# Optimization experiments

Hardware: AMD Instinct MI355X
Metric: run time of the kernel (lower is better)

Reference implementation:

```python
import jax, jax.numpy as jnp
import numpy as np

N_CLASS, N_SUPPORT, N_QUERY = 5, 5, 15
C, T, V = 128, 8, 25
LN_EPS = 1e-12


def setup_inputs() -> dict:
    key = jax.random.key(0)
    ks = jax.random.split(key, 6)
    n_tot = N_CLASS * (N_SUPPORT + N_QUERY)
    inp = jax.random.normal(ks[0], (n_tot, C, T, V), dtype=jnp.float32)
    # episode labels: 20 consecutive samples per class (arange // per_class)
    target = (jnp.arange(n_tot, dtype=jnp.int32) // (N_SUPPORT + N_QUERY)).astype(jnp.int32)
    s = 0.02
    p = lambda k: jax.random.normal(k, (C, C), dtype=jnp.float32) * s
    return {
        'input': inp,
        'Wq': p(ks[1]), 'bq': jnp.zeros((C,), jnp.float32),
        'Wk': p(ks[2]), 'bk': jnp.zeros((C,), jnp.float32),
        'Wv': p(ks[3]), 'bv': jnp.zeros((C,), jnp.float32),
        'Wo': p(ks[4]), 'bo': jnp.zeros((C,), jnp.float32),
        'ln_g': jnp.ones((C,), jnp.float32), 'ln_b': jnp.zeros((C,), jnp.float32),
        'target': target,
        'n_support': N_SUPPORT,
    }


def _layer_norm(x, g, b):
    mu = x.mean(-1, keepdims=True)
    var = ((x - mu) ** 2).mean(-1, keepdims=True)
    return (x - mu) * jax.lax.rsqrt(var + LN_EPS) * g + b


def _episode_forward(input, Wq, bq, Wk, bk, Wv, bv, Wo, bo, ln_g, ln_b, target, n_support):
    n_tot, c, t, v = input.shape
    m = N_CLASS
    per_class = n_tot // m
    n_query = per_class - n_support
    n = m * n_query

    # support/query split (stable argsort == torch.where per class for sorted labels)
    order = jnp.argsort(target).reshape(m, per_class)
    supp_idx = order[:, :n_support]                      # (m, h)
    qry_idx = order[:, n_support:].reshape(-1)           # (n,)
    z_proto = input[supp_idx]                            # (m, h, c, t, v)
    zq = input[qry_idx]                                  # (n, c, t, v)

    # ---- hal(): pairwise cross-attention over the vertex axis ----
    mh = m * n_support
    zq_p = jnp.transpose(zq, (0, 2, 3, 1))                                   # (n, t, v, c)
    zp_p = jnp.transpose(z_proto.reshape(mh, c, t, v), (0, 2, 3, 1))          # (mh, t, v, c)
    cat = jnp.concatenate([zq_p, zp_p], axis=0)                               # (n1, t, v, c)
    n1 = cat.shape[0]

    # Q from each of the n1 items, K/V from each of the mh prototypes.
    # Equivalent to the original expand->reshape pairing, without duplicating K/V.
    Q = cat @ Wq + bq                                                         # (n1, t, v, c)
    K = zp_p @ Wk + bk                                                        # (mh, t, v, c)
    Vv = zp_p @ Wv + bv                                                       # (mh, t, v, c)
    scale = 1.0 / jnp.sqrt(jnp.asarray(c, dtype=Q.dtype))
    scores = jnp.einsum('ntqc,mtkc->nmtqk', Q, K) * scale                     # (n1, mh, t, v, v)
    attn = jax.nn.softmax(scores, axis=-1)
    ctx = jnp.einsum('nmtqk,mtkc->nmtqc', attn, Vv)                           # (n1, mh, t, v, c)
    out = _layer_norm(ctx @ Wo + bo + cat[:, None], ln_g, ln_b)               # residual + LN
    att = out.mean(axis=1)                                                    # (n1, t, v, c) mean over mh pairs

    zq_att = jnp.transpose(att[:n], (0, 3, 1, 2))                             # (n, c, t, v)
    proto_att = att[n:].reshape(m, n_support, t, v, c).mean(axis=1)           # (m, t, v, c)
    proto_att = jnp.transpose(proto_att, (0, 3, 1, 2))                        # (m, c, t, v)

    # ---- squared-Euclidean metric on flattened features ----
    zq_f = zq_att.reshape(n, -1)
    zp_f = proto_att.reshape(m, -1)
    dist = jnp.sum((zq_f[:, None, :] - zp_f[None, :, :]) ** 2, axis=-1)       # (n, m)

    log_p_y = jax.nn.log_softmax(-dist, axis=1).reshape(m, n_query, m)
    cls = jnp.arange(m)
    loss = -log_p_y[cls[:, None], jnp.arange(n_query)[None, :], cls[:, None]].mean()
    y_hat = jnp.argmax(log_p_y, axis=2)
    acc = (y_hat == cls[:, None]).astype(jnp.float32).mean()
    return loss, acc


def reference(input, Wq, bq, Wk, bk, Wv, bv, Wo, bo, ln_g, ln_b, target, n_support):
    return _episode_forward(input, Wq, bq, Wk, bk, Wv, bv, Wo, bo, ln_g, ln_b, target, n_support)
```

## Files before the change

### kernel.cpp

```cpp
#include <hip/hip_runtime.h>
#include <math.h>

#define NTOT 100
#define NQ   75
#define NP   25
#define CC   128
#define TT   8
#define VV   25
#define NCLS 5
#define NSUP 5
#define NQRY 15
#define ROW  (TT*VV*CC)
#define TILE (VV*CC)
#define ROWS_Q 20000
#define ROWS_S 5000
#define RB_Q 625
#define RB_S 157

typedef __attribute__((ext_vector_type(8))) short short8;
typedef __attribute__((ext_vector_type(16))) float f32x16;

typedef union { uint4 u4; short8 s8; } pk_t;

__device__ __forceinline__ ushort f2bf(float f) {
    uint u = __float_as_uint(f);
    u += 0x7FFFu + ((u >> 16) & 1u);
    return (ushort)(u >> 16);
}
__device__ __forceinline__ float bf2f(uint u16v) {
    return __uint_as_float(u16v << 16);
}
__device__ __forceinline__ uint pkbf(float a, float b) {
    return (uint)f2bf(a) | ((uint)f2bf(b) << 16);
}

__global__ __launch_bounds__(256) void k_pack(
    const float* __restrict__ Wq, const float* __restrict__ Wk,
    const float* __restrict__ Wv, const float* __restrict__ Wo,
    const int* __restrict__ target,
    ushort* __restrict__ WfG, int* __restrict__ ordG) {
    int which = blockIdx.x;
    if (which == 4) {
        __shared__ int tg[NTOT];
        int tid = threadIdx.x;
        if (tid < NTOT) tg[tid] = target[tid];
        __syncthreads();
        if (tid < NTOT) {
            int ti = tg[tid], rank = 0;
            for (int j = 0; j < NTOT; ++j) {
                int tj = tg[j];
                rank += (tj < ti) || (tj == ti && j < tid);
            }
            ordG[rank] = tid;
        }
        return;
    }
    const float* W = (which == 0) ? Wq : (which == 1) ? Wk : (which == 2) ? Wv : Wo;
    ushort* dstbase = WfG + (size_t)which * 16384;
    for (int o = threadIdx.x; o < 2048; o += 256) {
        int k8 = o >> 7, c = o & 127;
        uint4 pk;
        pk.x = pkbf(W[(k8*8+0)*128 + c], W[(k8*8+1)*128 + c]);
        pk.y = pkbf(W[(k8*8+2)*128 + c], W[(k8*8+3)*128 + c]);
        pk.z = pkbf(W[(k8*8+4)*128 + c], W[(k8*8+5)*128 + c]);
        pk.w = pkbf(W[(k8*8+6)*128 + c], W[(k8*8+7)*128 + c]);
        int dst = (((c >> 5) * 8 + (k8 >> 1)) * 64 + ((c & 31) + 32 * (k8 & 1))) * 8;
        *(uint4*)(dstbase + dst) = pk;
    }
}

__global__ __launch_bounds__(256) void k_proj(
    const float* __restrict__ input, const int* __restrict__ ordG,
    const ushort* __restrict__ WfG,
    const float* __restrict__ bq, const float* __restrict__ bk,
    const float* __restrict__ bv,
    ushort* __restrict__ catC, ushort* __restrict__ Qf,
    ushort* __restrict__ Kf, ushort* __restrict__ Vf,
    int* __restrict__ counter) {
    __shared__ ushort stage[32 * 132];
    __shared__ ushort VtF[4096];

    int bid = blockIdx.x, tid = threadIdx.x;
    int w = tid >> 6, lane = tid & 63, half = lane >> 5, l31 = lane & 31;

    if (bid == 0 && tid == 0) *counter = 0;

    bool isQ = bid >= RB_S;
    int rowblk = isQ ? bid - RB_S : bid;
    int rlimit = isQ ? ROWS_Q : ROWS_S;
    int g0 = rowblk * 32;
    int gend = min(g0 + 32, rlimit);

    for (int nn = g0 / 200; nn <= (gend - 1) / 200; ++nn) {
        int lo = max(g0 - nn * 200, 0);
        int hi = min(gend - 1 - nn * 200, 199);
        int len = hi - lo + 1;
        int nidx = isQ ? nn : (NQ + nn);
        int src;
        if (nidx < NQ) { int m = nidx / NQRY, qq = nidx - m * NQRY; src = ordG[m * 20 + NSUP + qq]; }
        else           { int i2 = nidx - NQ; int m = i2 / NSUP, s = i2 - m * NSUP; src = ordG[m * 20 + s]; }
        const float* inb = input + (size_t)src * ROW + lo;
        int rbase = nn * 200 + lo - g0;
        int nv4 = len >> 2;
        int total4 = nv4 << 7;
        int qstep = 256 / nv4, rstep = 256 - qstep * nv4;
        int c = tid / nv4, v = tid - c * nv4;
        for (int idx = tid; idx < total4; idx += 256) {
            int k = v << 2;
            float4 f = *(const float4*)(inb + c * 200 + k);
            int ro = (rbase + k) * 132 + c;
            stage[ro]       = f2bf(f.x);
            stage[ro + 132] = f2bf(f.y);
            stage[ro + 264] = f2bf(f.z);
            stage[ro + 396] = f2bf(f.w);
            c += qstep; v += rstep;
            if (v >= nv4) { v -= nv4; ++c; }
        }
    }
    __syncthreads();

    short8 af[8];
    #pragma unroll
    for (int ks = 0; ks < 8; ++ks)
        af[ks] = *(const short8*)&stage[l31 * 132 + ks * 16 + half * 8];

    #define CHAIN(A, OUT, BASE) do {                                             \
        const ushort* bp_ = (BASE) + w * 4096 + lane * 8;                        \
        _Pragma("unroll")                                                        \
        for (int ks = 0; ks < 8; ++ks) {                                         \
            short8 bf_ = *(const short8*)(bp_ + ks * 512);                       \
            OUT = __builtin_amdgcn_mfma_f32_32x32x16_bf16(A[ks], bf_, OUT, 0, 0, 0); \
        }                                                                        \
    } while (0)

    if (isQ) {
        f32x16 Cm;
        #pragma unroll
        for (int r = 0; r < 16; ++r) Cm[r] = 0.f;
        CHAIN(af, Cm, WfG);
        float bcol = bq[w * 32 + l31];
        int c = w * 32 + l31;
        #pragma unroll
        for (int r = 0; r < 16; ++r) {
            int row = g0 + (r & 3) + 8 * (r >> 2) + 4 * half;
            int st = row / 25, vv = row - st * 25;
            size_t dst = (((size_t)st * 8 + (c >> 4)) * 64 + (vv + 32 * ((c >> 3) & 1))) * 8 + (c & 7);
            Qf[dst] = f2bf(Cm[r] + bcol);
        }
        uint* cc = (uint*)catC + (size_t)g0 * 64;
        for (int idx = tid; idx < 2048; idx += 256) {
            int row = idx >> 6, c2 = (idx & 63) * 2;
            cc[idx] = (uint)stage[row * 132 + c2] | ((uint)stage[row * 132 + c2 + 1] << 16);
        }
    } else {
        {
            f32x16 Cm;
            #pragma unroll
            for (int r = 0; r < 16; ++r) Cm[r] = 0.f;
            CHAIN(af, Cm, WfG + 16384);
            float bcol = bk[w * 32 + l31];
            int c = w * 32 + l31;
            #pragma unroll
            for (int r = 0; r < 16; ++r) {
                int row = g0 + (r & 3) + 8 * (r >> 2) + 4 * half;
                if (row < ROWS_S) {
                    int st = row / 25, vv = row - st * 25;
                    size_t dst = (((size_t)st * 8 + (c >> 4)) * 64 + (vv + 32 * ((c >> 3) & 1))) * 8 + (c & 7);
                    Kf[dst] = f2bf(Cm[r] + bcol);
                }
            }
        }
        {
            f32x16 Cm;
            #pragma unroll
            for (int r = 0; r < 16; ++r) Cm[r] = 0.f;
            CHAIN(af, Cm, WfG + 32768);
            float bcol = bv[w * 32 + l31];
            int c = w * 32 + l31;
            int ks2 = c >> 4, kh = (c >> 3) & 1, j2 = c & 7;
            #pragma unroll
            for (int r = 0; r < 16; ++r) {
                int rowLocal = (r & 3) + 8 * (r >> 2) + 4 * half;
                VtF[ks2 * 512 + (rowLocal + 32 * kh) * 8 + j2] = f2bf(Cm[r] + bcol);
            }
        }
        __syncthreads();
        short8 a2[8];
        #pragma unroll
        for (int ks = 0; ks < 8; ++ks)
            a2[ks] = *(const short8*)&VtF[ks * 512 + lane * 8];
        {
            f32x16 Cm;
            #pragma unroll
            for (int r = 0; r < 16; ++r) Cm[r] = 0.f;
            CHAIN(a2, Cm, WfG + 49152);
            int c = w * 32 + l31;
            #pragma unroll
            for (int r = 0; r < 16; ++r) {
                int row = g0 + (r & 3) + 8 * (r >> 2) + 4 * half;
                if (row < ROWS_S) {
                    int tile = row / 25, vv = row - tile * 25;
                    size_t dst = ((((size_t)tile * 4 + (c >> 5)) * 2 + (vv >> 4)) * 64
                                  + ((c & 31) + 32 * ((vv & 15) >> 3))) * 8 + (vv & 7);
                    Vf[dst] = f2bf(Cm[r]);
                }
            }
        }
    }
    #undef CHAIN
}

__global__ __launch_bounds__(256, 2) void k_attn(
    const ushort* __restrict__ Qf, const ushort* __restrict__ Kf,
    const ushort* __restrict__ Vf, const ushort* __restrict__ catC,
    const float* __restrict__ bo, float* __restrict__ att) {
    __shared__ __align__(16) char smem[26016];
    float*  catb = (float*)smem;
    ushort* qls  = (ushort*)(smem + 12912);
    float (*red)[50][65] = (float (*)[50][65])smem;

    int pair = blockIdx.x;
    int t = pair & 7;
    int tid = threadIdx.x;
    int wv = tid >> 6, lane = tid & 63;
    int q = lane & 31, half = lane >> 5;

    {
        const uint* cc = (const uint*)catC + (size_t)pair * 1600;
        for (int i2 = tid; i2 < 1600; i2 += 256) {
            uint u = cc[i2];
            int r = i2 >> 6, c2 = (i2 & 63) * 2;
            catb[r * 129 + c2]     = bf2f(u & 0xffffu) + bo[c2];
            catb[r * 129 + c2 + 1] = bf2f(u >> 16) + bo[c2 + 1];
        }
    }
    {
        const uint* qp = (const uint*)(Qf + (size_t)pair * 4096);
        uint* ql = (uint*)qls;
        for (int i2 = tid; i2 < 2048; i2 += 256) ql[i2] = qp[i2];
    }
    __syncthreads();

    int qc = q < 25 ? q : 24;
    float attsum[64];
    #pragma unroll
    for (int i = 0; i < 64; ++i) attsum[i] = 0.f;
    float Csc = 0.f;

    const float CEXP = (float)(1.4426950408889634 * 0.08838834764831845);

    const ushort* kbase = Kf + (size_t)t * 4096 + lane * 8;
    short8 kf[8];
    #pragma unroll
    for (int ks = 0; ks < 8; ++ks)
        kf[ks] = *(const short8*)(kbase + (size_t)wv * 32768 + ks * 512);

    int cnt = (wv == 0) ? 7 : 6;
    for (int mi = 0; mi < cnt; ++mi) {
        int m = wv + 4 * mi;

        f32x16 S;
        #pragma unroll
        for (int r = 0; r < 16; ++r) S[r] = 0.f;
        #pragma unroll
        for (int ks = 0; ks < 8; ++ks) {
            short8 qv = *(const short8*)(qls + ks * 512 + lane * 8);
            S = __builtin_amdgcn_mfma_f32_32x32x16_bf16(kf[ks], qv, S, 0, 0, 0);
        }

        float p[16], mx = -3e38f;
        #pragma unroll
        for (int r = 0; r < 16; ++r) {
            int key = (r & 3) + 8 * (r >> 2) + 4 * half;
            float v = (key < 25) ? S[r] : -3e38f;
            p[r] = v; mx = fmaxf(mx, v);
        }
        mx = fmaxf(mx, __shfl_xor(mx, 32));
        float sum = 0.f;
        #pragma unroll
        for (int r = 0; r < 16; ++r) { p[r] = exp2f((p[r] - mx) * CEXP); sum += p[r]; }
        sum += __shfl_xor(sum, 32);
        float inv = 1.f / sum;

        const ushort* vp = Vf + ((size_t)(m * 8 + t)) * 4096 + lane * 8;
        short8 vf0 = *(const short8*)(vp);
        short8 vf1 = *(const short8*)(vp + 512);
        short8 vf2 = *(const short8*)(vp + 1024);
        short8 vf3 = *(const short8*)(vp + 1536);
        short8 vf4 = *(const short8*)(vp + 2048);
        short8 vf5 = *(const short8*)(vp + 2560);
        short8 vf6 = *(const short8*)(vp + 3072);
        short8 vf7 = *(const short8*)(vp + 3584);
        #pragma unroll
        for (int ks = 0; ks < 8; ++ks)
            kf[ks] = *(const short8*)(kbase + (size_t)(m + 4) * 32768 + ks * 512);

        uint o01   = pkbf(p[0] * inv,  p[1] * inv);
        uint o23   = pkbf(p[2] * inv,  p[3] * inv);
        uint o45   = pkbf(p[4] * inv,  p[5] * inv);
        uint o67   = pkbf(p[6] * inv,  p[7] * inv);
        uint o89   = pkbf(p[8] * inv,  p[9] * inv);
        uint o1011 = pkbf(p[10] * inv, p[11] * inv);
        uint o1213 = pkbf(p[12] * inv, p[13] * inv);
        uint o1415 = pkbf(p[14] * inv, p[15] * inv);
        bool h0 = (half == 0);
        uint rA = __shfl_xor(h0 ? o45 : o01, 32);
        uint rB = __shfl_xor(h0 ? o67 : o23, 32);
        uint rC = __shfl_xor(h0 ? o1213 : o89, 32);
        uint rD = __shfl_xor(h0 ? o1415 : o1011, 32);
        pk_t P0, P1;
        P0.u4 = h0 ? make_uint4(o01, o23, rA, rB) : make_uint4(rA, rB, o45, o67);
        P1.u4 = h0 ? make_uint4(o89, o1011, rC, rD) : make_uint4(rC, rD, o1213, o1415);
        short8 pb0 = P0.s8, pb1 = P1.s8;

        f32x16 ctx[4];
        #pragma unroll
        for (int mt = 0; mt < 4; ++mt) {
            #pragma unroll
            for (int r = 0; r < 16; ++r) ctx[mt][r] = 0.f;
        }
        ctx[0] = __builtin_amdgcn_mfma_f32_32x32x16_bf16(vf0, pb0, ctx[0], 0, 0, 0);
        ctx[0] = __builtin_amdgcn_mfma_f32_32x32x16_bf16(vf1, pb1, ctx[0], 0, 0, 0);
        ctx[1] = __builtin_amdgcn_mfma_f32_32x32x16_bf16(vf2, pb0, ctx[1], 0, 0, 0);
        ctx[1] = __builtin_amdgcn_mfma_f32_32x32x16_bf16(vf3, pb1, ctx[1], 0, 0, 0);
        ctx[2] = __builtin_amdgcn_mfma_f32_32x32x16_bf16(vf4, pb0, ctx[2], 0, 0, 0);
        ctx[2] = __builtin_amdgcn_mfma_f32_32x32x16_bf16(vf5, pb1, ctx[2], 0, 0, 0);
        ctx[3] = __builtin_amdgcn_mfma_f32_32x32x16_bf16(vf6, pb0, ctx[3], 0, 0, 0);
        ctx[3] = __builtin_amdgcn_mfma_f32_32x32x16_bf16(vf7, pb1, ctx[3], 0, 0, 0);

        float s1 = 0.f, s2 = 0.f;
        #pragma unroll
        for (int mt = 0; mt < 4; ++mt) {
            float t1 = 0.f, t2 = 0.f;
            #pragma unroll
            for (int r = 0; r < 16; ++r) {
                int c = mt * 32 + (r & 3) + 8 * (r >> 2) + 4 * half;
                float xv = ctx[mt][r] + catb[qc * 129 + c];
                ctx[mt][r] = xv;
                t1 += xv; t2 = fmaf(xv, xv, t2);
            }
            s1 += t1; s2 += t2;
        }
        s1 += __shfl_xor(s1, 32); s2 += __shfl_xor(s2, 32);
        float mu = s1 * (1.f / 128.f);
        float var = s2 * (1.f / 128.f) - mu * mu;
        var = fmaxf(var, 0.f);
        float rs = rsqrtf(var + 1e-12f);
        #pragma unroll
        for (int i = 0; i < 64; ++i)
            attsum[i] = fmaf(ctx[i >> 4][i & 15], rs, attsum[i]);
        Csc = fmaf(-mu, rs, Csc);
    }

    __syncthreads();
    int s = half * 25 + q;
    bool act = q < 25;
    if ((wv == 1 || wv == 3) && act) {
        float (*rg)[65] = red[wv >> 1];
        #pragma unroll
        for (int i = 0; i < 64; ++i) rg[s][i] = attsum[i];
        rg[s][64] = Csc;
    }
    __syncthreads();
    if ((wv == 0 || wv == 2) && act) {
        float (*rg)[65] = red[wv >> 1];
        #pragma unroll
        for (int i = 0; i < 64; ++i) attsum[i] += rg[s][i];
        Csc += rg[s][64];
    }
    __syncthreads();
    if (wv == 2 && act) {
        #pragma unroll
        for (int i = 0; i < 64; ++i) red[0][s][i] = attsum[i];
        red[0][s][64] = Csc;
    }
    __syncthreads();
    if (wv == 0 && act) {
        #pragma unroll
        for (int i = 0; i < 64; ++i) attsum[i] += red[0][s][i];
        Csc += red[0][s][64];
        float* ap = att + (size_t)pair * TILE + q * 128;
        #pragma unroll
        for (int mt = 0; mt < 4; ++mt) {
            #pragma unroll
            for (int rg4 = 0; rg4 < 4; ++rg4) {
                int c0 = mt * 32 + 8 * rg4 + 4 * half;
                int i0 = mt * 16 + rg4 * 4;
                float4 o;
                o.x = attsum[i0 + 0] + Csc; o.y = attsum[i0 + 1] + Csc;
                o.z = attsum[i0 + 2] + Csc; o.w = attsum[i0 + 3] + Csc;
                *(float4*)&ap[c0] = o;
            }
        }
    }
}

__global__ __launch_bounds__(256) void k_proto(
    const float* __restrict__ att, float* __restrict__ proto) {
    int b = blockIdx.x;
    int j = b >> 3, chunk = b & 7;
    const float4* s0 = (const float4*)(att + (size_t)(NQ + j * 5 + 0) * ROW);
    const float4* s1 = (const float4*)(att + (size_t)(NQ + j * 5 + 1) * ROW);
    const float4* s2 = (const float4*)(att + (size_t)(NQ + j * 5 + 2) * ROW);
    const float4* s3 = (const float4*)(att + (size_t)(NQ + j * 5 + 3) * ROW);
    const float4* s4 = (const float4*)(att + (size_t)(NQ + j * 5 + 4) * ROW);
    float4* pr = (float4*)(proto + (size_t)j * ROW);
    int e0 = chunk * 800, e1 = e0 + 800;
    for (int e4 = e0 + threadIdx.x; e4 < e1; e4 += 256) {
        float4 q0 = s0[e4], q1 = s1[e4], q2 = s2[e4], q3 = s3[e4], q4 = s4[e4];
        float4 o;
        o.x = 0.2f * (q0.x + q1.x + q2.x + q3.x + q4.x);
        o.y = 0.2f * (q0.y + q1.y + q2.y + q3.y + q4.y);
        o.z = 0.2f * (q0.z + q1.z + q2.z + q3.z + q4.z);
        o.w = 0.2f * (q0.w + q1.w + q2.w + q3.w + q4.w);
        pr[e4] = o;
    }
}

__global__ __launch_bounds__(256) void k_dist_loss(
    const float* __restrict__ att, const float* __restrict__ proto,
    const float* __restrict__ ln_g,
    float* __restrict__ dist, int* __restrict__ counter,
    float* __restrict__ out) {
    int i = blockIdx.x;
    const float4* a  = (const float4*)(att + (size_t)i * ROW);
    const float4* p0 = (const float4*)(proto + (size_t)0 * ROW);
    const float4* p1 = (const float4*)(proto + (size_t)1 * ROW);
    const float4* p2 = (const float4*)(proto + (size_t)2 * ROW);
    const float4* p3 = (const float4*)(proto + (size_t)3 * ROW);
    const float4* p4 = (const float4*)(proto + (size_t)4 * ROW);
    float d0 = 0.f, d1 = 0.f, d2 = 0.f, d3 = 0.f, d4 = 0.f;
    for (int e4 = threadIdx.x; e4 < 6400; e4 += 256) {
        float4 av = a[e4];
        float4 g4 = *(const float4*)(ln_g + (e4 & 31) * 4);
        float gx = g4.x * g4.x, gy = g4.y * g4.y, gz = g4.z * g4.z, gw = g4.w * g4.w;
        #define ACC(PD, DD) do {                                              \
            float4 pv = PD[e4];                                               \
            float dx = av.x - pv.x, dy = av.y - pv.y;                         \
            float dz = av.z - pv.z, dw = av.w - pv.w;                         \
            DD = fmaf(gx, dx * dx, DD);                                       \
            DD = fmaf(gy, dy * dy, DD);                                       \
            DD = fmaf(gz, dz * dz, DD);                                       \
            DD = fmaf(gw, dw * dw, DD);                                       \
        } while (0)
        ACC(p0, d0); ACC(p1, d1); ACC(p2, d2); ACC(p3, d3); ACC(p4, d4);
        #undef ACC
    }
    #pragma unroll
    for (int msk = 32; msk >= 1; msk >>= 1) {
        d0 += __shfl_xor(d0, msk);
        d1 += __shfl_xor(d1, msk);
        d2 += __shfl_xor(d2, msk);
        d3 += __shfl_xor(d3, msk);
        d4 += __shfl_xor(d4, msk);
    }
    __shared__ float part[4][5];
    __shared__ int lastFlag;
    int lane = threadIdx.x & 63, wv = threadIdx.x >> 6;
    if (lane == 0) {
        part[wv][0] = d0; part[wv][1] = d1; part[wv][2] = d2;
        part[wv][3] = d3; part[wv][4] = d4;
    }
    __syncthreads();
    if (threadIdx.x == 0) {
        #pragma unroll
        for (int j = 0; j < 5; ++j) {
            float total = (part[0][j] + part[1][j] + part[2][j] + part[3][j]) * (1.f / 625.f);
            __hip_atomic_store(&dist[i * 5 + j], total, __ATOMIC_RELEASE, __HIP_MEMORY_SCOPE_AGENT);
        }
        int tk = __hip_atomic_fetch_add(counter, 1, __ATOMIC_ACQ_REL, __HIP_MEMORY_SCOPE_AGENT);
        lastFlag = (tk == 74);
    }
    __syncthreads();
    if (!lastFlag) return;

    int iq = threadIdx.x;
    float li = 0.f, ok = 0.f;
    if (iq < NQ) {
        float dd[5];
        #pragma unroll
        for (int jj = 0; jj < 5; ++jj)
            dd[jj] = __hip_atomic_load(&dist[iq * 5 + jj], __ATOMIC_ACQUIRE, __HIP_MEMORY_SCOPE_AGENT);
        int cls = iq / NQRY;
        float mind = dd[0];
        int best = 0;
        #pragma unroll
        for (int jj = 1; jj < 5; ++jj) {
            if (dd[jj] < mind) mind = dd[jj];
            if (dd[jj] < dd[best]) best = jj;
        }
        float sume = 0.f;
        #pragma unroll
        for (int jj = 0; jj < 5; ++jj) sume += expf(mind - dd[jj]);
        float lse = logf(sume) - mind;
        li = dd[cls] + lse;
        ok = (best == cls) ? 1.f : 0.f;
    }
    #pragma unroll
    for (int msk = 32; msk >= 1; msk >>= 1) {
        li += __shfl_xor(li, msk);
        ok += __shfl_xor(ok, msk);
    }
    if (lane == 0) { part[wv][0] = li; part[wv][1] = ok; }
    __syncthreads();
    if (threadIdx.x == 0) {
        out[0] = (part[0][0] + part[1][0] + part[2][0] + part[3][0]) / 75.f;
        out[1] = (part[0][1] + part[1][1] + part[2][1] + part[3][1]) / 75.f;
    }
}

extern "C" void kernel_launch(void* const* d_in, const int* in_sizes, int n_in,
                              void* d_out, int out_size, void* d_ws, size_t ws_size,
                              hipStream_t stream) {
    const float* input = (const float*)d_in[0];
    const float* Wq   = (const float*)d_in[1];
    const float* bq   = (const float*)d_in[2];
    const float* Wk   = (const float*)d_in[3];
    const float* bk   = (const float*)d_in[4];
    const float* Wv   = (const float*)d_in[5];
    const float* bv   = (const float*)d_in[6];
    const float* Wo   = (const float*)d_in[7];
    const float* bo   = (const float*)d_in[8];
    const float* ln_g = (const float*)d_in[9];
    const float* ln_b = (const float*)d_in[10];
    const int* target = (const int*)d_in[11];
    float* out = (float*)d_out;
    (void)ln_b;

    float* ws = (float*)d_ws;
    ushort* catC = (ushort*)ws;
    ushort* Qf   = catC + 2560000;
    ushort* Kf   = Qf + 3276800;
    ushort* Vf   = Kf + 819200;
    float*  att  = (float*)(Vf + 819200);
    float*  distb = att + 2560000;
    int*    counter = (int*)(distb + 512);
    ushort* WfG  = (ushort*)(counter + 16);
    int*    ordG = (int*)(WfG + 65536);
    float*  proto = (float*)catC;

    k_pack<<<5, 256, 0, stream>>>(Wq, Wk, Wv, Wo, target, WfG, ordG);
    k_proj<<<RB_Q + RB_S, 256, 0, stream>>>(input, ordG, WfG, bq, bk, bv,
                                            catC, Qf, Kf, Vf, counter);
    k_attn<<<800, 256, 0, stream>>>(Qf, Kf, Vf, catC, bo, att);
    k_proto<<<40, 256, 0, stream>>>(att, proto);
    k_dist_loss<<<75, 256, 0, stream>>>(att, proto, ln_g, distb, counter, out);
}
```

Measured before the change: 170.1 us.

## Accumulate attention sums via LDS atomics and drop K-fragment prefetch

Each wave now adds its normalized context contributions into a shared-memory accumulator with atomicAdd, replacing the 64-register per-thread accumulator and the multi-step cross-wave tree reduction. K fragments are loaded at the top of each iteration instead of prefetched for the next one, and the final tile is written cooperatively by all threads. This frees registers, aiming at higher occupancy, but adds many LDS atomics per iteration, exposes K load latency, and raises LDS use per block.

```diff
diff --git a/kernel.cpp b/kernel.cpp
--- a/kernel.cpp
+++ b/kernel.cpp
@@ -214,10 +214,11 @@
     const ushort* __restrict__ Qf, const ushort* __restrict__ Kf,
     const ushort* __restrict__ Vf, const ushort* __restrict__ catC,
     const float* __restrict__ bo, float* __restrict__ att) {
-    __shared__ __align__(16) char smem[26016];
-    float*  catb = (float*)smem;
-    ushort* qls  = (ushort*)(smem + 12912);
-    float (*red)[50][65] = (float (*)[50][65])smem;
+    __shared__ __align__(16) char smem[37744];
+    float*  catb   = (float*)smem;
+    ushort* qls    = (ushort*)(smem + 12912);
+    float*  attacc = (float*)(smem + 21104);
+    float*  cscacc = attacc + 32 * 129;
 
     int pair = blockIdx.x;
     int t = pair & 7;
@@ -239,25 +240,24 @@
         uint* ql = (uint*)qls;
         for (int i2 = tid; i2 < 2048; i2 += 256) ql[i2] = qp[i2];
     }
+    for (int i2 = tid; i2 < 32 * 129 + 32; i2 += 256) attacc[i2] = 0.f;
     __syncthreads();
 
     int qc = q < 25 ? q : 24;
-    float attsum[64];
-    #pragma unroll
-    for (int i = 0; i < 64; ++i) attsum[i] = 0.f;
-    float Csc = 0.f;
+    bool act = q < 25;
 
     const float CEXP = (float)(1.4426950408889634 * 0.08838834764831845);
 
     const ushort* kbase = Kf + (size_t)t * 4096 + lane * 8;
-    short8 kf[8];
-    #pragma unroll
-    for (int ks = 0; ks < 8; ++ks)
-        kf[ks] = *(const short8*)(kbase + (size_t)wv * 32768 + ks * 512);
 
     int cnt = (wv == 0) ? 7 : 6;
     for (int mi = 0; mi < cnt; ++mi) {
         int m = wv + 4 * mi;
+
+        short8 kf[8];
+        #pragma unroll
+        for (int ks = 0; ks < 8; ++ks)
+            kf[ks] = *(const short8*)(kbase + (size_t)m * 32768 + ks * 512);
 
         f32x16 S;
         #pragma unroll
@@ -291,9 +291,6 @@
         short8 vf5 = *(const short8*)(vp + 2560);
         short8 vf6 = *(const short8*)(vp + 3072);
         short8 vf7 = *(const short8*)(vp + 3584);
-        #pragma unroll
-        for (int ks = 0; ks < 8; ++ks)
-            kf[ks] = *(const short8*)(kbase + (size_t)(m + 4) * 32768 + ks * 512);
 
         uint o01   = pkbf(p[0] * inv,  p[1] * inv);
         uint o23   = pkbf(p[2] * inv,  p[3] * inv);
@@ -346,51 +343,31 @@
         float var = s2 * (1.f / 128.f) - mu * mu;
         var = fmaxf(var, 0.f);
         float rs = rsqrtf(var + 1e-12f);
-        #pragma unroll
-        for (int i = 0; i < 64; ++i)
-            attsum[i] = fmaf(ctx[i >> 4][i & 15], rs, attsum[i]);
-        Csc = fmaf(-mu, rs, Csc);
+
+        if (act) {
+            float* arow = attacc + q * 129;
+            #pragma unroll
+            for (int mt = 0; mt < 4; ++mt) {
+                #pragma unroll
+                for (int r = 0; r < 16; ++r) {
+                    int c = mt * 32 + (r & 3) + 8 * (r >> 2) + 4 * half;
+                    atomicAdd(&arow[c], ctx[mt][r] * rs);
+                }
+            }
+            if (h0) atomicAdd(&cscacc[q], -mu * rs);
+        }
     }
 
     __syncthreads();
-    int s = half * 25 + q;
-    bool act = q < 25;
-    if ((wv == 1 || wv == 3) && act) {
-        float (*rg)[65] = red[wv >> 1];
-        #pragma unroll
-        for (int i = 0; i < 64; ++i) rg[s][i] = attsum[i];
-        rg[s][64] = Csc;
-    }
-    __syncthreads();
-    if ((wv == 0 || wv == 2) && act) {
-        float (*rg)[65] = red[wv >> 1];
-        #pragma unroll
-        for (int i = 0; i < 64; ++i) attsum[i] += rg[s][i];
-        Csc += rg[s][64];
-    }
-    __syncthreads();
-    if (wv == 2 && act) {
-        #pragma unroll
-        for (int i = 0; i < 64; ++i) red[0][s][i] = attsum[i];
-        red[0][s][64] = Csc;
-    }
-    __syncthreads();
-    if (wv == 0 && act) {
-        #pragma unroll
-        for (int i = 0; i < 64; ++i) attsum[i] += red[0][s][i];
-        Csc += red[0][s][64];
-        float* ap = att + (size_t)pair * TILE + q * 128;
-        #pragma unroll
-        for (int mt = 0; mt < 4; ++mt) {
-            #pragma unroll
-            for (int rg4 = 0; rg4 < 4; ++rg4) {
-                int c0 = mt * 32 + 8 * rg4 + 4 * half;
-                int i0 = mt * 16 + rg4 * 4;
-                float4 o;
-                o.x = attsum[i0 + 0] + Csc; o.y = attsum[i0 + 1] + Csc;
-                o.z = attsum[i0 + 2] + Csc; o.w = attsum[i0 + 3] + Csc;
-                *(float4*)&ap[c0] = o;
-            }
+    {
+        float* ap = att + (size_t)pair * TILE;
+        for (int idx = tid; idx < 800; idx += 256) {
+            int qq = idx >> 5, c4 = (idx & 31) * 4;
+            float cs = cscacc[qq];
+            const float* ar = attacc + qq * 129 + c4;
+            float4 o;
+            o.x = ar[0] + cs; o.y = ar[1] + cs; o.z = ar[2] + cs; o.w = ar[3] + cs;
+            *(float4*)&ap[qq * 128 + c4] = o;
         }
     }
 }
```

Result: slower. 549.7 us (+223.1%).

## Fuse Q projection and input staging into attention kernel

Applied to the files above, without the earlier changes.

The Q projection and the bf16 staging of each (item, t) tile move from k_proj into k_attn, which now reads the fp32 input directly, transposes it into shared memory, and computes Q with MFMA locally. k_proj now handles only the support rows (K, V and the Wo-folded V), so its grid shrinks from 782 to 157 blocks. This removes the global round-trip of the Qf and catC intermediates. In exchange k_attn uses more shared memory and does an uncoalesced strided transpose load from the input for each block.

```diff
diff --git a/kernel.cpp b/kernel.cpp
--- a/kernel.cpp
+++ b/kernel.cpp
@@ -12,9 +12,7 @@
 #define NQRY 15
 #define ROW  (TT*VV*CC)
 #define TILE (VV*CC)
-#define ROWS_Q 20000
 #define ROWS_S 5000
-#define RB_Q 625
 #define RB_S 157
 
 typedef __attribute__((ext_vector_type(8))) short short8;
@@ -72,9 +70,7 @@
 __global__ __launch_bounds__(256) void k_proj(
     const float* __restrict__ input, const int* __restrict__ ordG,
     const ushort* __restrict__ WfG,
-    const float* __restrict__ bq, const float* __restrict__ bk,
-    const float* __restrict__ bv,
-    ushort* __restrict__ catC, ushort* __restrict__ Qf,
+    const float* __restrict__ bk, const float* __restrict__ bv,
     ushort* __restrict__ Kf, ushort* __restrict__ Vf,
     int* __restrict__ counter) {
     __shared__ ushort stage[32 * 132];
@@ -85,20 +81,15 @@
 
     if (bid == 0 && tid == 0) *counter = 0;
 
-    bool isQ = bid >= RB_S;
-    int rowblk = isQ ? bid - RB_S : bid;
-    int rlimit = isQ ? ROWS_Q : ROWS_S;
-    int g0 = rowblk * 32;
-    int gend = min(g0 + 32, rlimit);
+    int g0 = bid * 32;
+    int gend = min(g0 + 32, ROWS_S);
 
     for (int nn = g0 / 200; nn <= (gend - 1) / 200; ++nn) {
         int lo = max(g0 - nn * 200, 0);
         int hi = min(gend - 1 - nn * 200, 199);
         int len = hi - lo + 1;
-        int nidx = isQ ? nn : (NQ + nn);
-        int src;
-        if (nidx < NQ) { int m = nidx / NQRY, qq = nidx - m * NQRY; src = ordG[m * 20 + NSUP + qq]; }
-        else           { int i2 = nidx - NQ; int m = i2 / NSUP, s = i2 - m * NSUP; src = ordG[m * 20 + s]; }
+        int m = nn / NSUP, s = nn - m * NSUP;
+        int src = ordG[m * 20 + s];
         const float* inb = input + (size_t)src * ROW + lo;
         int rbase = nn * 200 + lo - g0;
         int nv4 = len >> 2;
@@ -133,111 +124,119 @@
         }                                                                        \
     } while (0)
 
-    if (isQ) {
+    {
         f32x16 Cm;
         #pragma unroll
         for (int r = 0; r < 16; ++r) Cm[r] = 0.f;
-        CHAIN(af, Cm, WfG);
-        float bcol = bq[w * 32 + l31];
+        CHAIN(af, Cm, WfG + 16384);
+        float bcol = bk[w * 32 + l31];
         int c = w * 32 + l31;
         #pragma unroll
         for (int r = 0; r < 16; ++r) {
             int row = g0 + (r & 3) + 8 * (r >> 2) + 4 * half;
-            int st = row / 25, vv = row - st * 25;
-            size_t dst = (((size_t)st * 8 + (c >> 4)) * 64 + (vv + 32 * ((c >> 3) & 1))) * 8 + (c & 7);
-            Qf[dst] = f2bf(Cm[r] + bcol);
-        }
-        uint* cc = (uint*)catC + (size_t)g0 * 64;
-        for (int idx = tid; idx < 2048; idx += 256) {
-            int row = idx >> 6, c2 = (idx & 63) * 2;
-            cc[idx] = (uint)stage[row * 132 + c2] | ((uint)stage[row * 132 + c2 + 1] << 16);
-        }
-    } else {
-        {
-            f32x16 Cm;
-            #pragma unroll
-            for (int r = 0; r < 16; ++r) Cm[r] = 0.f;
-            CHAIN(af, Cm, WfG + 16384);
-            float bcol = bk[w * 32 + l31];
-            int c = w * 32 + l31;
-            #pragma unroll
-            for (int r = 0; r < 16; ++r) {
-                int row = g0 + (r & 3) + 8 * (r >> 2) + 4 * half;
-                if (row < ROWS_S) {
-                    int st = row / 25, vv = row - st * 25;
-                    size_t dst = (((size_t)st * 8 + (c >> 4)) * 64 + (vv + 32 * ((c >> 3) & 1))) * 8 + (c & 7);
-                    Kf[dst] = f2bf(Cm[r] + bcol);
-                }
+            if (row < ROWS_S) {
+                int st = row / 25, vv = row - st * 25;
+                size_t dst = (((size_t)st * 8 + (c >> 4)) * 64 + (vv + 32 * ((c >> 3) & 1))) * 8 + (c & 7);
+                Kf[dst] = f2bf(Cm[r] + bcol);
             }
         }
-        {
-            f32x16 Cm;
-            #pragma unroll
-            for (int r = 0; r < 16; ++r) Cm[r] = 0.f;
-            CHAIN(af, Cm, WfG + 32768);
-            float bcol = bv[w * 32 + l31];
-            int c = w * 32 + l31;
-            int ks2 = c >> 4, kh = (c >> 3) & 1, j2 = c & 7;
-            #pragma unroll
-            for (int r = 0; r < 16; ++r) {
-                int rowLocal = (r & 3) + 8 * (r >> 2) + 4 * half;
-                VtF[ks2 * 512 + (rowLocal + 32 * kh) * 8 + j2] = f2bf(Cm[r] + bcol);
+    }
+    {
+        f32x16 Cm;
+        #pragma unroll
+        for (int r = 0; r < 16; ++r) Cm[r] = 0.f;
+        CHAIN(af, Cm, WfG + 32768);
+        float bcol = bv[w * 32 + l31];
+        int c = w * 32 + l31;
+        int ks2 = c >> 4, kh = (c >> 3) & 1, j2 = c & 7;
+        #pragma unroll
+        for (int r = 0; r < 16; ++r) {
+            int rowLocal = (r & 3) + 8 * (r >> 2) + 4 * half;
+            VtF[ks2 * 512 + (rowLocal + 32 * kh) * 8 + j2] = f2bf(Cm[r] + bcol);
+        }
+    }
+    __syncthreads();
+    short8 a2[8];
+    #pragma unroll
+    for (int ks = 0; ks < 8; ++ks)
+        a2[ks] = *(const short8*)&VtF[ks * 512 + lane * 8];
+    {
+        f32x16 Cm;
+        #pragma unroll
+        for (int r = 0; r < 16; ++r) Cm[r] = 0.f;
+        CHAIN(a2, Cm, WfG + 49152);
+        int c = w * 32 + l31;
+        #pragma unroll
+        for (int r = 0; r < 16; ++r) {
+            int row = g0 + (r & 3) + 8 * (r >> 2) + 4 * half;
+            if (row < ROWS_S) {
+                int tile = row / 25, vv = row - tile * 25;
+                size_t dst = ((((size_t)tile * 4 + (c >> 5)) * 2 + (vv >> 4)) * 64
+                              + ((c & 31) + 32 * ((vv & 15) >> 3))) * 8 + (vv & 7);
+                Vf[dst] = f2bf(Cm[r]);
             }
         }
-        __syncthreads();
-        short8 a2[8];
-        #pragma unroll
-        for (int ks = 0; ks < 8; ++ks)
-            a2[ks] = *(const short8*)&VtF[ks * 512 + lane * 8];
-        {
-            f32x16 Cm;
-            #pragma unroll
-            for (int r = 0; r < 16; ++r) Cm[r] = 0.f;
-            CHAIN(a2, Cm, WfG + 49152);
-            int c = w * 32 + l31;
-            #pragma unroll
-            for (int r = 0; r < 16; ++r) {
-                int row = g0 + (r & 3) + 8 * (r >> 2) + 4 * half;
-                if (row < ROWS_S) {
-                    int tile = row / 25, vv = row - tile * 25;
-                    size_t dst = ((((size_t)tile * 4 + (c >> 5)) * 2 + (vv >> 4)) * 64
-                                  + ((c & 31) + 32 * ((vv & 15) >> 3))) * 8 + (vv & 7);
-                    Vf[dst] = f2bf(Cm[r]);
-                }
-            }
-        }
     }
     #undef CHAIN
 }
 
 __global__ __launch_bounds__(256, 2) void k_attn(
-    const ushort* __restrict__ Qf, const ushort* __restrict__ Kf,
-    const ushort* __restrict__ Vf, const ushort* __restrict__ catC,
+    const float* __restrict__ input, const int* __restrict__ ordG,
+    const ushort* __restrict__ WfG, const float* __restrict__ bq,
+    const ushort* __restrict__ Kf, const ushort* __restrict__ Vf,
     const float* __restrict__ bo, float* __restrict__ att) {
-    __shared__ __align__(16) char smem[26016];
-    float*  catb = (float*)smem;
-    ushort* qls  = (ushort*)(smem + 12912);
+    __shared__ __align__(16) char smem[29552];
+    float*  catb  = (float*)smem;
+    ushort* qls   = (ushort*)(smem + 12912);
+    ushort* stage = (ushort*)(smem + 21104);
     float (*red)[50][65] = (float (*)[50][65])smem;
 
     int pair = blockIdx.x;
-    int t = pair & 7;
+    int t = pair & 7, n = pair >> 3;
     int tid = threadIdx.x;
     int wv = tid >> 6, lane = tid & 63;
-    int q = lane & 31, half = lane >> 5;
-
+    int q = lane & 31, half = lane >> 5, l31 = lane & 31;
+
+    int src;
+    if (n < NQ) { int m = n / NQRY, qq = n - m * NQRY; src = ordG[m * 20 + NSUP + qq]; }
+    else        { int i2 = n - NQ; int m = i2 / NSUP, s = i2 - m * NSUP; src = ordG[m * 20 + s]; }
+
+    for (int idx = tid; idx < 7 * 132; idx += 256) stage[3300 + idx] = 0;
     {
-        const uint* cc = (const uint*)catC + (size_t)pair * 1600;
-        for (int i2 = tid; i2 < 1600; i2 += 256) {
-            uint u = cc[i2];
-            int r = i2 >> 6, c2 = (i2 & 63) * 2;
-            catb[r * 129 + c2]     = bf2f(u & 0xffffu) + bo[c2];
-            catb[r * 129 + c2 + 1] = bf2f(u >> 16) + bo[c2 + 1];
-        }
+        const float* inb = input + (size_t)src * ROW + t * 25;
+        for (int idx = tid; idx < 3200; idx += 256) {
+            int c = idx / 25, v = idx - c * 25;
+            stage[v * 132 + c] = f2bf(inb[c * 200 + v]);
+        }
+    }
+    __syncthreads();
+
+    for (int idx = tid; idx < 3200; idx += 256) {
+        int r = idx >> 7, c2 = idx & 127;
+        catb[r * 129 + c2] = bf2f((uint)stage[r * 132 + c2]) + bo[c2];
     }
     {
-        const uint* qp = (const uint*)(Qf + (size_t)pair * 4096);
-        uint* ql = (uint*)qls;
-        for (int i2 = tid; i2 < 2048; i2 += 256) ql[i2] = qp[i2];
+        short8 af[8];
+        #pragma unroll
+        for (int ks = 0; ks < 8; ++ks)
+            af[ks] = *(const short8*)&stage[l31 * 132 + ks * 16 + half * 8];
+        f32x16 Cm;
+        #pragma unroll
+        for (int r = 0; r < 16; ++r) Cm[r] = 0.f;
+        const ushort* bp = WfG + wv * 4096 + lane * 8;
+        #pragma unroll
+        for (int ks = 0; ks < 8; ++ks) {
+            short8 bf_ = *(const short8*)(bp + ks * 512);
+            Cm = __builtin_amdgcn_mfma_f32_32x32x16_bf16(af[ks], bf_, Cm, 0, 0, 0);
+        }
+        float bcol = bq[wv * 32 + l31];
+        int c = wv * 32 + l31;
+        int ks2 = c >> 4, kh = (c >> 3) & 1, j2 = c & 7;
+        #pragma unroll
+        for (int r = 0; r < 16; ++r) {
+            int rowLocal = (r & 3) + 8 * (r >> 2) + 4 * half;
+            qls[ks2 * 512 + (rowLocal + 32 * kh) * 8 + j2] = f2bf(Cm[r] + bcol);
+        }
     }
     __syncthreads();
 
@@ -528,21 +527,18 @@
     (void)ln_b;
 
     float* ws = (float*)d_ws;
-    ushort* catC = (ushort*)ws;
-    ushort* Qf   = catC + 2560000;
-    ushort* Kf   = Qf + 3276800;
+    float*  proto = (float*)ws;
+    ushort* Kf   = (ushort*)(proto + 5 * ROW);
     ushort* Vf   = Kf + 819200;
     float*  att  = (float*)(Vf + 819200);
     float*  distb = att + 2560000;
     int*    counter = (int*)(distb + 512);
     ushort* WfG  = (ushort*)(counter + 16);
     int*    ordG = (int*)(WfG + 65536);
-    float*  proto = (float*)catC;
 
     k_pack<<<5, 256, 0, stream>>>(Wq, Wk, Wv, Wo, target, WfG, ordG);
-    k_proj<<<RB_Q + RB_S, 256, 0, stream>>>(input, ordG, WfG, bq, bk, bv,
-                                            catC, Qf, Kf, Vf, counter);
-    k_attn<<<800, 256, 0, stream>>>(Qf, Kf, Vf, catC, bo, att);
+    k_proj<<<RB_S, 256, 0, stream>>>(input, ordG, WfG, bk, bv, Kf, Vf, counter);
+    k_attn<<<800, 256, 0, stream>>>(input, ordG, WfG, bq, Kf, Vf, bo, att);
     k_proto<<<40, 256, 0, stream>>>(att, proto);
     k_dist_loss<<<75, 256, 0, stream>>>(att, proto, ln_g, distb, counter, out);
 }
```

Measured after the change: 174.6 us. 2.6% more time.
